# Performance work log

Measured on AMD Instinct MI355X. Metric: run time of the kernel, lower is better.

Reference implementation:

```python
import jax, jax.numpy as jnp
import numpy as np

N = 1048576          # nodes at current depth (children), divisible by 8
M = N // 8           # non-empty parent nodes (conv outputs)
NNUM_PARENT = 262144 # total parent nodes at depth-1
C_IN = 128
C_OUT = 256


def setup_inputs() -> dict:
    key = jax.random.key(0)
    k1, k2, k3 = jax.random.split(key, 3)
    data = jax.random.normal(k1, (N, C_IN), dtype=jnp.float32)
    weights = jax.random.normal(k2, (8, C_IN, C_OUT), dtype=jnp.float32) * (1.0 / np.sqrt(8 * C_IN))
    # sorted unique positions of non-empty parents within [0, NNUM_PARENT)
    perm = jax.random.permutation(k3, NNUM_PARENT)
    nempty_idx = jnp.sort(perm[:M]).astype(jnp.int32)
    return {"data": data, "weights": weights, "nempty_idx": nempty_idx,
            "nnum_parent": NNUM_PARENT}


def reference(data, weights, nempty_idx, nnum_parent):
    # kernel-2 stride-2 conv: each consecutive group of 8 children -> one parent
    c_in, c_out = weights.shape[1], weights.shape[2]
    out = data.reshape(-1, 8 * c_in) @ weights.reshape(8 * c_in, c_out)  # [M, C_out]
    # octree_pad at depth-1: scatter into all parent nodes, zeros at empty ones
    full = jnp.zeros((nnum_parent, c_out), dtype=out.dtype).at[nempty_idx].set(out)
    return full
```

## Files before the change

kernel.cpp:

```cpp
#include <hip/hip_runtime.h>
#include <hip/hip_bf16.h>

typedef float f32x4 __attribute__((ext_vector_type(4)));
typedef short s16x8 __attribute__((ext_vector_type(8)));

using bf16 = __hip_bfloat16;

namespace {
constexpr int KD = 1024;
constexpr int BM = 128;
constexpr int BK = 32;
constexpr int NT = KD / BK;
}

__device__ __forceinline__ int swz_slot(int row, int c) {
  return (row ^ ((row >> 2) & 1)) * 4 + (c ^ (row & 3));
}
__device__ __forceinline__ void swz_inv(int s, int& row, int& c) {
  int rp = s >> 2, x = s & 3;
  row = rp ^ ((rp >> 2) & 1);
  c = x ^ (row & 3);
}

__device__ __forceinline__ s16x8 cvt8(f32x4 a, f32x4 b) {
  union { s16x8 v; bf16 h[8]; } u;
#pragma unroll
  for (int j = 0; j < 4; ++j) u.h[j] = __float2bfloat16(a[j]);
#pragma unroll
  for (int j = 0; j < 4; ++j) u.h[j + 4] = __float2bfloat16(b[j]);
  return u.v;
}

__global__ void k_transpose_w(const float* __restrict__ w, bf16* __restrict__ bt) {
  int t = blockIdx.x * 256 + threadIdx.x;
  int n = t & 255;
  int k0 = (t >> 8) << 3;
  union { s16x8 v; bf16 h[8]; } u;
#pragma unroll
  for (int j = 0; j < 8; ++j)
    u.h[j] = __float2bfloat16(w[(size_t)(k0 + j) * 256 + n]);
  *(s16x8*)(bt + (size_t)n * KD + k0) = u.v;
}

__global__ void k_clear_flags(int* __restrict__ flags, int np4) {
  int i = blockIdx.x * 256 + threadIdx.x;
  if (i < np4) ((int4*)flags)[i] = make_int4(0, 0, 0, 0);
}

__global__ void k_set_flags(const int* __restrict__ idx, int* __restrict__ flags, int m) {
  int i = blockIdx.x * 256 + threadIdx.x;
  if (i < m) flags[idx[i]] = 1;
}

__global__ void k_zero_empty(const int* __restrict__ flags, float* __restrict__ out) {
  int row = blockIdx.x * 4 + (threadIdx.x >> 6);
  int lane = threadIdx.x & 63;
  if (flags[row] == 0) {
    f32x4 z = {0.f, 0.f, 0.f, 0.f};
    *(f32x4*)(out + (size_t)row * 256 + lane * 4) = z;
  }
}

__global__ __launch_bounds__(512, 4)
void k_gemm(const float* __restrict__ A, const bf16* __restrict__ Bt,
            const int* __restrict__ idx, float* __restrict__ out) {
  __shared__ bf16 As[2][BM * BK];
  __shared__ bf16 Bs[2][256 * BK];

  const int tid = threadIdx.x;
  const int lane = tid & 63;
  const int wave = tid >> 6;
  const int wm = wave >> 2;
  const int wn = wave & 3;
  const int m0 = blockIdx.x * BM;

  const int ar = tid >> 2;
  const int ac = tid & 3;
  const float* aptr = A + (size_t)(m0 + ar) * KD + ac * 8;
  const int a_w_off = swz_slot(ar, ac) * 8;

  int bn0, bc0, bn1, bc1;
  swz_inv(tid, bn0, bc0);
  swz_inv(512 + tid, bn1, bc1);
  const bf16* bp0 = Bt + (size_t)bn0 * KD + bc0 * 8;
  const bf16* bp1 = Bt + (size_t)bn1 * KD + bc1 * 8;
  const int b_w_off0 = tid * 8;
  const int b_w_off1 = (512 + tid) * 8;

  const int arow = wm * 64 + (lane & 15);
  const int kc = lane >> 4;
  const int a_r_off = swz_slot(arow, kc) * 8;
  const int brow = wn * 64 + (lane & 15);
  const int b_r_off = swz_slot(brow, kc) * 8;

  f32x4 acc[4][4] = {};

  {
    f32x4 a0 = *(const f32x4*)aptr;
    f32x4 a1 = *(const f32x4*)(aptr + 4);
    s16x8 b0 = *(const s16x8*)bp0;
    s16x8 b1 = *(const s16x8*)bp1;
    *(s16x8*)(&As[0][a_w_off]) = cvt8(a0, a1);
    *(s16x8*)(&Bs[0][b_w_off0]) = b0;
    *(s16x8*)(&Bs[0][b_w_off1]) = b1;
  }
  __syncthreads();

  int cur = 0;
#pragma unroll 1
  for (int t = 0; t < NT; ++t) {
    f32x4 na0, na1;
    s16x8 nb0, nb1;
    const bool pf = (t + 1 < NT);
    if (pf) {
      const float* ap = aptr + (t + 1) * BK;
      na0 = *(const f32x4*)ap;
      na1 = *(const f32x4*)(ap + 4);
      nb0 = *(const s16x8*)(bp0 + (t + 1) * BK);
      nb1 = *(const s16x8*)(bp1 + (t + 1) * BK);
    }

    s16x8 af[4], bfr[4];
#pragma unroll
    for (int fm = 0; fm < 4; ++fm)
      af[fm] = *(const s16x8*)(&As[cur][a_r_off + fm * 512]);
#pragma unroll
    for (int fn = 0; fn < 4; ++fn)
      bfr[fn] = *(const s16x8*)(&Bs[cur][b_r_off + fn * 512]);

#pragma unroll
    for (int fm = 0; fm < 4; ++fm)
#pragma unroll
      for (int fn = 0; fn < 4; ++fn)
        acc[fm][fn] = __builtin_amdgcn_mfma_f32_16x16x32_bf16(
            af[fm], bfr[fn], acc[fm][fn], 0, 0, 0);

    if (pf) {
      int nxt = cur ^ 1;
      *(s16x8*)(&As[nxt][a_w_off]) = cvt8(na0, na1);
      *(s16x8*)(&Bs[nxt][b_w_off0]) = nb0;
      *(s16x8*)(&Bs[nxt][b_w_off1]) = nb1;
      cur = nxt;
    }
    __syncthreads();
  }

  const int col0 = wn * 64 + (lane & 15);
  const int rb = m0 + wm * 64 + ((lane >> 4) << 2);
#pragma unroll
  for (int fm = 0; fm < 4; ++fm) {
#pragma unroll
    for (int j = 0; j < 4; ++j) {
      int orow = idx[rb + fm * 16 + j];
      float* op = out + (size_t)orow * 256 + col0;
#pragma unroll
      for (int fn = 0; fn < 4; ++fn)
        op[fn * 16] = acc[fm][fn][j];
    }
  }
}

extern "C" void kernel_launch(void* const* d_in, const int* in_sizes, int n_in,
                              void* d_out, int out_size, void* d_ws, size_t ws_size,
                              hipStream_t stream) {
  const float* data = (const float*)d_in[0];
  const float* w    = (const float*)d_in[1];
  const int*   idx  = (const int*)d_in[2];
  float* out = (float*)d_out;

  const int M  = in_sizes[2];
  const int NP = out_size / 256;

  int* flags = (int*)d_ws;
  bf16* bt = (bf16*)((char*)d_ws + (size_t)NP * sizeof(int));

  k_transpose_w<<<128, 256, 0, stream>>>(w, bt);
  k_clear_flags<<<(NP / 4 + 255) / 256, 256, 0, stream>>>(flags, NP / 4);
  k_set_flags<<<(M + 255) / 256, 256, 0, stream>>>(idx, flags, M);
  k_zero_empty<<<NP / 4, 256, 0, stream>>>(flags, out);
  k_gemm<<<M / BM, 512, 0, stream>>>(data, bt, idx, out);
}
```

Measured before the change: 235.6 us.

## Use direct global-to-LDS loads for GEMM tiles and fuse zero-fill into GEMM launch

Replaces register-staged global loads with global_load_lds async copies into shared memory. A tiles are now kept as fp32 in LDS and converted to bf16 at fragment-read time, with new XOR swizzles for A and B. The separate zero-fill kernel for empty parent rows is folded into the GEMM launch as extra blocks, dropping one launch and letting the zeroing overlap the GEMM. In exchange, the fp32 A tile doubles LDS use, and the bf16 conversion is now repeated by each wave that reads the same rows.

```diff
diff --git a/kernel.cpp b/kernel.cpp
--- a/kernel.cpp
+++ b/kernel.cpp
@@ -11,15 +11,15 @@
 constexpr int BM = 128;
 constexpr int BK = 32;
 constexpr int NT = KD / BK;
+constexpr int MBLK = 131072 / BM;
+constexpr int ZBLK = 1024;
 }
 
-__device__ __forceinline__ int swz_slot(int row, int c) {
-  return (row ^ ((row >> 2) & 1)) * 4 + (c ^ (row & 3));
-}
-__device__ __forceinline__ void swz_inv(int s, int& row, int& c) {
-  int rp = s >> 2, x = s & 3;
-  row = rp ^ ((rp >> 2) & 1);
-  c = x ^ (row & 3);
+typedef __attribute__((address_space(1))) const void GVoid;
+typedef __attribute__((address_space(3))) void LVoid;
+
+__device__ __forceinline__ void gld16(const void* g, void* l) {
+  __builtin_amdgcn_global_load_lds((GVoid*)g, (LVoid*)l, 16, 0, 0);
 }
 
 __device__ __forceinline__ s16x8 cvt8(f32x4 a, f32x4 b) {
@@ -52,97 +52,87 @@
   if (i < m) flags[idx[i]] = 1;
 }
 
-__global__ void k_zero_empty(const int* __restrict__ flags, float* __restrict__ out) {
-  int row = blockIdx.x * 4 + (threadIdx.x >> 6);
-  int lane = threadIdx.x & 63;
-  if (flags[row] == 0) {
-    f32x4 z = {0.f, 0.f, 0.f, 0.f};
-    *(f32x4*)(out + (size_t)row * 256 + lane * 4) = z;
-  }
-}
-
 __global__ __launch_bounds__(512, 4)
-void k_gemm(const float* __restrict__ A, const bf16* __restrict__ Bt,
-            const int* __restrict__ idx, float* __restrict__ out) {
-  __shared__ bf16 As[2][BM * BK];
-  __shared__ bf16 Bs[2][256 * BK];
+void k_fused(const float* __restrict__ A, const bf16* __restrict__ Bt,
+             const int* __restrict__ idx, const int* __restrict__ flags,
+             float* __restrict__ out, int NP) {
+  __shared__ float As[2][BM * BK];
+  __shared__ bf16  Bs[2][256 * BK];
 
   const int tid = threadIdx.x;
   const int lane = tid & 63;
   const int wave = tid >> 6;
+
+  if (blockIdx.x >= MBLK) {
+    const int zb = blockIdx.x - MBLK;
+    f32x4 z = {0.f, 0.f, 0.f, 0.f};
+    for (int row = zb * 8 + wave; row < NP; row += ZBLK * 8) {
+      if (flags[row] == 0)
+        *(f32x4*)(out + (size_t)row * 256 + lane * 4) = z;
+    }
+    return;
+  }
+
+  const int m0 = blockIdx.x * BM;
   const int wm = wave >> 2;
   const int wn = wave & 3;
-  const int m0 = blockIdx.x * BM;
 
-  const int ar = tid >> 2;
-  const int ac = tid & 3;
-  const float* aptr = A + (size_t)(m0 + ar) * KD + ac * 8;
-  const int a_w_off = swz_slot(ar, ac) * 8;
+  const int as0 = tid, as1 = 512 + tid;
+  const int ar0 = as0 >> 3, ac0 = (as0 & 7) ^ (ar0 & 6);
+  const int ar1 = as1 >> 3, ac1 = (as1 & 7) ^ (ar1 & 6);
+  const float* aSrc0 = A + (size_t)(m0 + ar0) * KD + ac0 * 4;
+  const float* aSrc1 = A + (size_t)(m0 + ar1) * KD + ac1 * 4;
+  const int aOff0 = (wave * 64) * 4;
+  const int aOff1 = (512 + wave * 64) * 4;
 
-  int bn0, bc0, bn1, bc1;
-  swz_inv(tid, bn0, bc0);
-  swz_inv(512 + tid, bn1, bc1);
-  const bf16* bp0 = Bt + (size_t)bn0 * KD + bc0 * 8;
-  const bf16* bp1 = Bt + (size_t)bn1 * KD + bc1 * 8;
-  const int b_w_off0 = tid * 8;
-  const int b_w_off1 = (512 + tid) * 8;
+  const int bs0 = tid, bs1 = 512 + tid;
+  const int br0 = bs0 >> 2, bc0 = (bs0 & 3) ^ (br0 & 3);
+  const int br1 = bs1 >> 2, bc1 = (bs1 & 3) ^ (br1 & 3);
+  const bf16* bSrc0 = Bt + (size_t)br0 * KD + bc0 * 8;
+  const bf16* bSrc1 = Bt + (size_t)br1 * KD + bc1 * 8;
+  const int bOff0 = (wave * 64) * 8;
+  const int bOff1 = (512 + wave * 64) * 8;
 
   const int arow = wm * 64 + (lane & 15);
   const int kc = lane >> 4;
-  const int a_r_off = swz_slot(arow, kc) * 8;
+  const int aRd = arow * 32 + (((2 * kc) ^ (arow & 6)) * 4);
   const int brow = wn * 64 + (lane & 15);
-  const int b_r_off = swz_slot(brow, kc) * 8;
+  const int bRd = brow * 32 + ((kc ^ (brow & 3)) * 8);
 
   f32x4 acc[4][4] = {};
 
-  {
-    f32x4 a0 = *(const f32x4*)aptr;
-    f32x4 a1 = *(const f32x4*)(aptr + 4);
-    s16x8 b0 = *(const s16x8*)bp0;
-    s16x8 b1 = *(const s16x8*)bp1;
-    *(s16x8*)(&As[0][a_w_off]) = cvt8(a0, a1);
-    *(s16x8*)(&Bs[0][b_w_off0]) = b0;
-    *(s16x8*)(&Bs[0][b_w_off1]) = b1;
-  }
+  auto stage = [&](int buf, int t) {
+    gld16(aSrc0 + t * BK, &As[buf][aOff0]);
+    gld16(aSrc1 + t * BK, &As[buf][aOff1]);
+    gld16(bSrc0 + t * BK, &Bs[buf][bOff0]);
+    gld16(bSrc1 + t * BK, &Bs[buf][bOff1]);
+  };
+
+  stage(0, 0);
   __syncthreads();
 
   int cur = 0;
 #pragma unroll 1
   for (int t = 0; t < NT; ++t) {
-    f32x4 na0, na1;
-    s16x8 nb0, nb1;
-    const bool pf = (t + 1 < NT);
-    if (pf) {
-      const float* ap = aptr + (t + 1) * BK;
-      na0 = *(const f32x4*)ap;
-      na1 = *(const f32x4*)(ap + 4);
-      nb0 = *(const s16x8*)(bp0 + (t + 1) * BK);
-      nb1 = *(const s16x8*)(bp1 + (t + 1) * BK);
-    }
+    if (t + 1 < NT) stage(cur ^ 1, t + 1);
 
-    s16x8 af[4], bfr[4];
-#pragma unroll
-    for (int fm = 0; fm < 4; ++fm)
-      af[fm] = *(const s16x8*)(&As[cur][a_r_off + fm * 512]);
+    s16x8 bfr[4];
 #pragma unroll
     for (int fn = 0; fn < 4; ++fn)
-      bfr[fn] = *(const s16x8*)(&Bs[cur][b_r_off + fn * 512]);
+      bfr[fn] = *(const s16x8*)(&Bs[cur][bRd + fn * 512]);
 
 #pragma unroll
-    for (int fm = 0; fm < 4; ++fm)
+    for (int fm = 0; fm < 4; ++fm) {
+      f32x4 lo = *(const f32x4*)(&As[cur][aRd + fm * 512]);
+      f32x4 hi = *(const f32x4*)(&As[cur][aRd + fm * 512 + 4]);
+      s16x8 af = cvt8(lo, hi);
 #pragma unroll
       for (int fn = 0; fn < 4; ++fn)
         acc[fm][fn] = __builtin_amdgcn_mfma_f32_16x16x32_bf16(
-            af[fm], bfr[fn], acc[fm][fn], 0, 0, 0);
-
-    if (pf) {
-      int nxt = cur ^ 1;
-      *(s16x8*)(&As[nxt][a_w_off]) = cvt8(na0, na1);
-      *(s16x8*)(&Bs[nxt][b_w_off0]) = nb0;
-      *(s16x8*)(&Bs[nxt][b_w_off1]) = nb1;
-      cur = nxt;
+            af, bfr[fn], acc[fm][fn], 0, 0, 0);
     }
     __syncthreads();
+    cur ^= 1;
   }
 
   const int col0 = wn * 64 + (lane & 15);
@@ -177,6 +167,5 @@
   k_transpose_w<<<128, 256, 0, stream>>>(w, bt);
   k_clear_flags<<<(NP / 4 + 255) / 256, 256, 0, stream>>>(flags, NP / 4);
   k_set_flags<<<(M + 255) / 256, 256, 0, stream>>>(idx, flags, M);
-  k_zero_empty<<<NP / 4, 256, 0, stream>>>(flags, out);
-  k_gemm<<<M / BM, 512, 0, stream>>>(data, bt, idx, out);
+  k_fused<<<MBLK + ZBLK, 512, 0, stream>>>(data, bt, idx, flags, out, NP);
 }
```

After: 253.0 us. +7.4%, slower.
